# Kernel optimization log

Measured on AMD Instinct MI355X. Metric: run time of the kernel, lower is better.

Reference implementation:

```python
import jax, jax.numpy as jnp
from jax import lax
import numpy as np

B, C, H, W = 8, 256, 192, 192
ATT_K = 11
BN_EPS = 1e-5


def _dwconv(x, w, pad, stride=1):
    # x: NCHW, w: (C,1,kh,kw) depthwise
    return lax.conv_general_dilated(
        x, w, window_strides=(stride, stride), padding=pad,
        feature_group_count=x.shape[1],
        dimension_numbers=('NCHW', 'OIHW', 'NCHW'))


def _max_pool_3x3(x):
    return lax.reduce_window(x, -jnp.inf, lax.max,
                             (1, 1, 3, 3), (1, 1, 1, 1), 'SAME')


def _blur_pool(x, stride=3):
    # antialiased_cnns.BlurPool, filt_size=4: reflect pad [1,2,1,2], binomial 4x4, depthwise, stride 3
    c = x.shape[1]
    a = jnp.array([1., 3., 3., 1.], dtype=x.dtype)
    filt = (a[:, None] * a[None, :])
    filt = filt / jnp.sum(filt)
    w = jnp.tile(filt[None, None], (c, 1, 1, 1))  # (C,1,4,4)
    xp = jnp.pad(x, ((0, 0), (0, 0), (1, 2), (1, 2)), mode='reflect')
    return _dwconv(xp, w, 'VALID', stride=stride)


def _h_transform(x):
    b, c, h, w = x.shape
    x = jnp.pad(x, ((0, 0), (0, 0), (0, 0), (0, w)))
    x = x.reshape(b, c, -1)[..., :-w]
    return x.reshape(b, c, h, 2 * w - 1)


def _inv_h_transform(x):
    b, c, h, _ = x.shape  # last dim = 2h-1 (requires square)
    x = x.reshape(b, c, -1)
    x = jnp.pad(x, ((0, 0), (0, 0), (0, h)))
    x = x.reshape(b, c, h, 2 * h)
    return x[..., :h]


def _v_transform(x):
    return jnp.transpose(_h_transform(jnp.transpose(x, (0, 1, 3, 2))), (0, 1, 3, 2))


def _inv_v_transform(x):
    return jnp.transpose(_inv_h_transform(jnp.transpose(x, (0, 1, 3, 2))), (0, 1, 3, 2))


def setup_inputs() -> dict:
    key = jax.random.key(0)
    ks = jax.random.split(key, 5)
    pad = ATT_K // 2
    return {
        'x': jax.random.normal(ks[0], (B, C, H, W), dtype=jnp.float32),
        'w_h1': jax.random.normal(ks[1], (C, 1, ATT_K, 3), dtype=jnp.float32) * 0.1,
        'w_v1': jax.random.normal(ks[2], (C, 1, 3, ATT_K), dtype=jnp.float32) * 0.1,
        'w_h2': jax.random.normal(ks[3], (C, 1, ATT_K, 3), dtype=jnp.float32) * 0.1,
        'w_v2': jax.random.normal(ks[4], (C, 1, 3, ATT_K), dtype=jnp.float32) * 0.1,
        'bn_gamma': jnp.ones((C,), dtype=jnp.float32),
        'bn_beta': jnp.zeros((C,), dtype=jnp.float32),
        'bn_mean': jnp.zeros((C,), dtype=jnp.float32),
        'bn_var': jnp.ones((C,), dtype=jnp.float32),
    }


def reference(x, w_h1, w_v1, w_h2, w_v2, bn_gamma, bn_beta, bn_mean, bn_var):
    pad = ATT_K // 2
    b, c, h, w = x.shape

    x_tem = _max_pool_3x3(x)
    x_tem = _blur_pool(x_tem, stride=3)  # (B,C,64,64)

    x_h1 = _dwconv(x_tem, w_h1, ((pad, pad), (1, 1)))
    x_w1 = _dwconv(x_tem, w_v1, ((1, 1), (pad, pad)))

    # h == w (192 == 192): diagonal branch active
    x_h2 = _inv_h_transform(_dwconv(_h_transform(x_tem), w_h2, ((pad, pad), (1, 1))))
    x_w2 = _inv_v_transform(_dwconv(_v_transform(x_tem), w_v2, ((1, 1), (pad, pad))))

    s = x_h1 + x_w1 + x_h2 + x_w2
    # inference BatchNorm2d
    inv = bn_gamma / jnp.sqrt(bn_var + BN_EPS)
    att = (s - bn_mean[None, :, None, None]) * inv[None, :, None, None] + bn_beta[None, :, None, None]

    gate = jax.nn.sigmoid(att)
    # nearest interpolate to (h, w): idx = floor(i * in/out)
    ah, aw = gate.shape[2], gate.shape[3]
    idx_h = (jnp.arange(h) * ah) // h
    idx_w = (jnp.arange(w) * aw) // w
    gate_up = gate[:, :, idx_h][:, :, :, idx_w]

    return x[:, :c] * gate_up
```

## Files before the change

### kernel.cpp

```cpp
#include <hip/hip_runtime.h>
#include <hip/hip_fp16.h>
#include <math.h>

#define BN_EPS 1e-5f

typedef _Float16 f16x8 __attribute__((ext_vector_type(8)));
typedef float    f32x4 __attribute__((ext_vector_type(4)));

__device__ __forceinline__ float max3f(float a, float b, float c) {
    return fmaxf(fmaxf(a, b), c);
}

__global__ __launch_bounds__(512, 8)
void mra_fused(const float* __restrict__ x,
               const float* __restrict__ wh1,
               const float* __restrict__ wv1,
               const float* __restrict__ wh2,
               const float* __restrict__ wv2,
               const float* __restrict__ bng,
               const float* __restrict__ bnb,
               const float* __restrict__ bnm,
               const float* __restrict__ bnv,
               float* __restrict__ out)
{
    __shared__ __align__(16) __half sxp_h[76][88];
    __shared__ __align__(16) __half gate_h[64][72];
    __shared__ __align__(16) __half Tpad[13][48];

    const int plane = blockIdx.x;
    const int c     = plane & 255;
    const int tid   = threadIdx.x;
    const int lane  = tid & 63;
    const int w     = tid >> 6;
    const float* __restrict__ xp = x   + (size_t)plane * 36864;
    float* __restrict__       op = out + (size_t)plane * 36864;

    {
        int* z = (int*)&sxp_h[0][0];
        const int nInt = (76 * 88 * 2) / 4;
        #pragma unroll
        for (int i = 0; i < 7; ++i) {
            const int idx = tid + (i << 9);
            if (idx < nInt) z[idx] = 0;
        }
    }
    {
        const float* __restrict__ wh1p = wh1 + c * 33;
        const float* __restrict__ wv1p = wv1 + c * 33;
        const float* __restrict__ wh2p = wh2 + c * 33;
        const float* __restrict__ wv2p = wv2 + c * 33;
        for (int s = tid; s < 13 * 48; s += 512) {
            const int er = s / 48;
            const int e  = er - 6;
            const int d  = (s - er * 48) - 24;
            float t = 0.f;
            if (e >= -5 && e <= 5 && d >= -1 && d <= 1)
                t += wh1p[(e + 5) * 3 + d + 1];
            if (e >= -5 && e <= 5 && d + e >= -1 && d + e <= 1)
                t += wh2p[(e + 5) * 3 + d + e + 1];
            if (e >= -1 && e <= 1 && d >= -5 && d <= 5)
                t += wv1p[(e + 1) * 11 + d + 5];
            if (d + e >= -1 && d + e <= 1 && d >= -5 && d <= 5)
                t += wv2p[(d + e + 1) * 11 + d + 5];
            Tpad[er][s - er * 48] = __float2half(t);
        }
    }
    __syncthreads();

    {
        const int P0  = w << 3;
        const int r0  = 3 * P0 - 2;
        const int col = 3 * lane;

        float c0r[4], c1r[4], c2r[4];
        auto issue = [&](int k, int s) {
            int r = r0 + k;
            r = r < 0 ? 0 : (r > 191 ? 191 : r);
            const float* rp = xp + r * 192 + col;
            c0r[s] = rp[0]; c1r[s] = rp[1]; c2r[s] = rp[2];
        };
        issue(0, 0); issue(1, 1); issue(2, 2); issue(3, 3);

        float h[3][4];
        float hb[3];
        float hbp = 0.f;

        #pragma unroll
        for (int k = 0; k < 27; ++k) {
            const int s = k & 3;
            const float cc0 = c0r[s], cc1 = c1r[s], cc2 = c2r[s];
            if (k + 4 < 27) issue(k + 4, s);

            float xm2 = __shfl_up(cc1, 1);
            float xm1 = __shfl_up(cc2, 1);
            float xp3 = __shfl_down(cc0, 1);
            if (lane == 0)  xm1 = cc0;
            if (lane == 63) xp3 = cc2;

            const float hm_m1 = max3f(xm2, xm1, cc0);
            const float hm_0  = max3f(xm1, cc0, cc1);
            const float hm_1  = max3f(cc0, cc1, cc2);
            const float hm_2  = max3f(cc1, cc2, xp3);

            float* hk = h[k % 3];
            hk[0] = (lane == 0) ? hm_1 : hm_m1;
            hk[1] = hm_0; hk[2] = hm_1; hk[3] = hm_2;

            if (k >= 2) {
                const float* a = h[(k - 2) % 3];
                const float* b = h[(k - 1) % 3];
                const float* d = h[k % 3];
                const float e4 =
                      0.125f * max3f(a[0], b[0], d[0])
                    + 0.375f * max3f(a[1], b[1], d[1])
                    + 0.375f * max3f(a[2], b[2], d[2])
                    + 0.125f * max3f(a[3], b[3], d[3]);
                if (k == 2) {
                    hbp = e4;
                } else {
                    hb[k % 3] = e4;
                    if (k % 3 == 2) {
                        const int i = (k - 5) / 3;
                        float a_out;
                        if (i == 0 && w == 0)
                            a_out = 0.375f * hb[0] + 0.5f * hb[1] + 0.125f * hb[2];
                        else
                            a_out = 0.125f * hbp + 0.375f * hb[0]
                                  + 0.375f * hb[1] + 0.125f * hb[2];
                        hbp = hb[2];
                        sxp_h[(w << 3) + i + 6][lane + 8] = __float2half(a_out);
                    }
                }
            }
        }
    }
    __syncthreads();

    {
        const int lr = lane & 15;
        const int lg = lane >> 4;
        const int t0 = 2 * w;
        const int P0 = (t0 >> 2) << 4;
        const int Q0a = (t0 & 3) << 4;
        const int Q0b = ((t0 + 1) & 3) << 4;
        const int tb = lg * 8 + 16 - lr;

        f32x4 acc0 = {0.f, 0.f, 0.f, 0.f};
        f32x4 acc1 = {0.f, 0.f, 0.f, 0.f};

        #pragma unroll
        for (int e = -6; e <= 6; ++e) {
            const __half* trow = &Tpad[e + 6][0];
            f16x8 bf;
            #pragma unroll
            for (int j = 0; j < 8; ++j)
                bf[j] = *(const _Float16*)&trow[tb + j];
            const int row = P0 + lr + e + 6;
            const f16x8 a0 = *(const f16x8*)&sxp_h[row][Q0a + lg * 8];
            const f16x8 a1 = *(const f16x8*)&sxp_h[row][Q0b + lg * 8];
            acc0 = __builtin_amdgcn_mfma_f32_16x16x32_f16(a0, bf, acc0, 0, 0, 0);
            acc1 = __builtin_amdgcn_mfma_f32_16x16x32_f16(a1, bf, acc1, 0, 0, 0);
        }

        const float inv = bng[c] * rsqrtf(bnv[c] + BN_EPS);
        const float mu  = bnm[c];
        const float bt  = bnb[c];
        #pragma unroll
        for (int r = 0; r < 4; ++r) {
            const int gr = P0 + lg * 4 + r;
            const float g0 = 1.0f / (1.0f + __expf(-((acc0[r] - mu) * inv + bt)));
            const float g1 = 1.0f / (1.0f + __expf(-((acc1[r] - mu) * inv + bt)));
            gate_h[gr][Q0a + lr] = __float2half(g0);
            gate_h[gr][Q0b + lr] = __float2half(g1);
        }
    }
    __syncthreads();

    const float4* __restrict__ x4 = (const float4*)xp + w * 1152;
    float4* __restrict__       o4 = (float4*)op       + w * 1152;
    int rlj[3], gcj[3], rrj[3];
    #pragma unroll
    for (int j = 0; j < 3; ++j) {
        const int idx0 = lane + (j << 6);
        const int rw   = idx0 / 48;
        const int c4   = idx0 - rw * 48;
        rlj[j] = rw;
        const int jb = c4 << 2;
        gcj[j] = jb / 3;
        rrj[j] = jb - 3 * gcj[j];
    }
    #pragma unroll
    for (int u = 0; u < 6; ++u) {
        #pragma unroll
        for (int j = 0; j < 3; ++j) {
            const int row_l = rlj[j] + (u << 2);
            const int idx   = lane + ((u * 3 + j) << 6);
            const int gr    = (w << 3) + row_l / 3;
            const float g0 = __half2float(gate_h[gr][gcj[j]]);
            const float g1 = __half2float(gate_h[gr][gcj[j] + 1]);
            const float4 xv = x4[idx];
            float4 ov;
            const float s1 = (rrj[j] == 2) ? g1 : g0;
            const float s2 = (rrj[j] >= 1) ? g1 : g0;
            ov.x = xv.x * g0;
            ov.y = xv.y * s1;
            ov.z = xv.z * s2;
            ov.w = xv.w * g1;
            o4[idx] = ov;
        }
    }
}

extern "C" void kernel_launch(void* const* d_in, const int* in_sizes, int n_in,
                              void* d_out, int out_size, void* d_ws, size_t ws_size,
                              hipStream_t stream) {
    const float* x   = (const float*)d_in[0];
    const float* wh1 = (const float*)d_in[1];
    const float* wv1 = (const float*)d_in[2];
    const float* wh2 = (const float*)d_in[3];
    const float* wv2 = (const float*)d_in[4];
    const float* g   = (const float*)d_in[5];
    const float* b   = (const float*)d_in[6];
    const float* m   = (const float*)d_in[7];
    const float* v   = (const float*)d_in[8];

    mra_fused<<<dim3(8 * 256), dim3(512), 0, stream>>>(
        x, wh1, wv1, wh2, wv2, g, b, m, v, (float*)d_out);
}
```

Before: 163.8 us.

## Split fused kernel into gate-compute and gate-apply kernels via workspace

Splits the single fused kernel into two. The first computes the pooled conv gates per plane and writes them as fp16 to a global workspace. The second kernel reloads those gates and multiplies them over x, visiting planes in reverse order so the most recently read planes are more likely still in cache. The aim is to decouple the compute-heavy gate phase from the bandwidth-bound apply phase, at the cost of an extra launch, a workspace round-trip, and reading x twice. The old fused kernel stays as a fallback when the workspace is too small.

```diff
diff --git a/kernel.cpp b/kernel.cpp
--- a/kernel.cpp
+++ b/kernel.cpp
@@ -12,7 +12,7 @@
 }
 
 __global__ __launch_bounds__(512, 8)
-void mra_fused(const float* __restrict__ x,
+void mra_gates(const float* __restrict__ x,
                const float* __restrict__ wh1,
                const float* __restrict__ wv1,
                const float* __restrict__ wh2,
@@ -21,10 +21,10 @@
                const float* __restrict__ bnb,
                const float* __restrict__ bnm,
                const float* __restrict__ bnv,
-               float* __restrict__ out)
+               uint32_t* __restrict__ gws)
 {
     __shared__ __align__(16) __half sxp_h[76][88];
-    __shared__ __align__(16) __half gate_h[64][72];
+    __shared__ __align__(16) __half gate_d[64][64];
     __shared__ __align__(16) __half Tpad[13][48];
 
     const int plane = blockIdx.x;
@@ -32,8 +32,7 @@
     const int tid   = threadIdx.x;
     const int lane  = tid & 63;
     const int w     = tid >> 6;
-    const float* __restrict__ xp = x   + (size_t)plane * 36864;
-    float* __restrict__       op = out + (size_t)plane * 36864;
+    const float* __restrict__ xp = x + (size_t)plane * 36864;
 
     {
         int* z = (int*)&sxp_h[0][0];
@@ -140,10 +139,238 @@
         const int lr = lane & 15;
         const int lg = lane >> 4;
         const int t0 = 2 * w;
-        const int P0 = (t0 >> 2) << 4;
+        const int P0  = (t0 >> 2) << 4;
         const int Q0a = (t0 & 3) << 4;
         const int Q0b = ((t0 + 1) & 3) << 4;
-        const int tb = lg * 8 + 16 - lr;
+        const int tb  = lg * 8 + 16 - lr;
+
+        f32x4 acc0 = {0.f, 0.f, 0.f, 0.f};
+        f32x4 acc1 = {0.f, 0.f, 0.f, 0.f};
+
+        #pragma unroll
+        for (int e = -6; e <= 6; ++e) {
+            const __half* trow = &Tpad[e + 6][0];
+            f16x8 bf;
+            #pragma unroll
+            for (int j = 0; j < 8; ++j)
+                bf[j] = *(const _Float16*)&trow[tb + j];
+            const int row = P0 + lr + e + 6;
+            const f16x8 a0 = *(const f16x8*)&sxp_h[row][Q0a + lg * 8];
+            const f16x8 a1 = *(const f16x8*)&sxp_h[row][Q0b + lg * 8];
+            acc0 = __builtin_amdgcn_mfma_f32_16x16x32_f16(a0, bf, acc0, 0, 0, 0);
+            acc1 = __builtin_amdgcn_mfma_f32_16x16x32_f16(a1, bf, acc1, 0, 0, 0);
+        }
+
+        const float inv = bng[c] * rsqrtf(bnv[c] + BN_EPS);
+        const float mu  = bnm[c];
+        const float bt  = bnb[c];
+        #pragma unroll
+        for (int r = 0; r < 4; ++r) {
+            const int gr = P0 + lg * 4 + r;
+            const float g0 = 1.0f / (1.0f + __expf(-((acc0[r] - mu) * inv + bt)));
+            const float g1 = 1.0f / (1.0f + __expf(-((acc1[r] - mu) * inv + bt)));
+            gate_d[gr][Q0a + lr] = __float2half(g0);
+            gate_d[gr][Q0b + lr] = __float2half(g1);
+        }
+    }
+    __syncthreads();
+
+    {
+        const uint32_t* gu = (const uint32_t*)&gate_d[0][0];
+        uint32_t* gp = gws + (size_t)plane * 2048;
+        #pragma unroll
+        for (int i = 0; i < 4; ++i) gp[tid + (i << 9)] = gu[tid + (i << 9)];
+    }
+}
+
+__global__ __launch_bounds__(256, 8)
+void mra_apply(const float* __restrict__ x,
+               const uint32_t* __restrict__ gws,
+               float* __restrict__ out)
+{
+    __shared__ __align__(16) __half gate_l[64][64];
+
+    const int plane = 2047 - blockIdx.x;
+    const int tid   = threadIdx.x;
+    const float* __restrict__ xp = x   + (size_t)plane * 36864;
+    float* __restrict__       op = out + (size_t)plane * 36864;
+
+    {
+        uint32_t* gl = (uint32_t*)&gate_l[0][0];
+        const uint32_t* gp = gws + (size_t)plane * 2048;
+        #pragma unroll
+        for (int i = 0; i < 8; ++i) gl[tid + (i << 8)] = gp[tid + (i << 8)];
+    }
+    __syncthreads();
+
+    const float4* __restrict__ x4 = (const float4*)xp;
+    float4* __restrict__       o4 = (float4*)op;
+    int rowj[3], gcj[3], rrj[3];
+    #pragma unroll
+    for (int j = 0; j < 3; ++j) {
+        const int idx0 = tid + (j << 8);
+        const int rw   = idx0 / 48;
+        const int c4   = idx0 - rw * 48;
+        rowj[j] = rw;
+        const int jb = c4 << 2;
+        gcj[j] = jb / 3;
+        rrj[j] = jb - 3 * gcj[j];
+    }
+    #pragma unroll
+    for (int m = 0; m < 12; ++m) {
+        #pragma unroll
+        for (int j = 0; j < 3; ++j) {
+            const int row = rowj[j] + (m << 4);
+            const int idx = tid + ((m * 3 + j) << 8);
+            const int gr  = row / 3;
+            const float g0 = __half2float(gate_l[gr][gcj[j]]);
+            const float g1 = __half2float(gate_l[gr][gcj[j] + 1]);
+            const float4 xv = x4[idx];
+            float4 ov;
+            const float s1 = (rrj[j] == 2) ? g1 : g0;
+            const float s2 = (rrj[j] >= 1) ? g1 : g0;
+            ov.x = xv.x * g0;
+            ov.y = xv.y * s1;
+            ov.z = xv.z * s2;
+            ov.w = xv.w * g1;
+            o4[idx] = ov;
+        }
+    }
+}
+
+__global__ __launch_bounds__(512, 8)
+void mra_fused(const float* __restrict__ x,
+               const float* __restrict__ wh1,
+               const float* __restrict__ wv1,
+               const float* __restrict__ wh2,
+               const float* __restrict__ wv2,
+               const float* __restrict__ bng,
+               const float* __restrict__ bnb,
+               const float* __restrict__ bnm,
+               const float* __restrict__ bnv,
+               float* __restrict__ out)
+{
+    __shared__ __align__(16) __half sxp_h[76][88];
+    __shared__ __align__(16) __half gate_h[64][72];
+    __shared__ __align__(16) __half Tpad[13][48];
+
+    const int plane = blockIdx.x;
+    const int c     = plane & 255;
+    const int tid   = threadIdx.x;
+    const int lane  = tid & 63;
+    const int w     = tid >> 6;
+    const float* __restrict__ xp = x   + (size_t)plane * 36864;
+    float* __restrict__       op = out + (size_t)plane * 36864;
+
+    {
+        int* z = (int*)&sxp_h[0][0];
+        const int nInt = (76 * 88 * 2) / 4;
+        #pragma unroll
+        for (int i = 0; i < 7; ++i) {
+            const int idx = tid + (i << 9);
+            if (idx < nInt) z[idx] = 0;
+        }
+    }
+    {
+        const float* __restrict__ wh1p = wh1 + c * 33;
+        const float* __restrict__ wv1p = wv1 + c * 33;
+        const float* __restrict__ wh2p = wh2 + c * 33;
+        const float* __restrict__ wv2p = wv2 + c * 33;
+        for (int s = tid; s < 13 * 48; s += 512) {
+            const int er = s / 48;
+            const int e  = er - 6;
+            const int d  = (s - er * 48) - 24;
+            float t = 0.f;
+            if (e >= -5 && e <= 5 && d >= -1 && d <= 1)
+                t += wh1p[(e + 5) * 3 + d + 1];
+            if (e >= -5 && e <= 5 && d + e >= -1 && d + e <= 1)
+                t += wh2p[(e + 5) * 3 + d + e + 1];
+            if (e >= -1 && e <= 1 && d >= -5 && d <= 5)
+                t += wv1p[(e + 1) * 11 + d + 5];
+            if (d + e >= -1 && d + e <= 1 && d >= -5 && d <= 5)
+                t += wv2p[(d + e + 1) * 11 + d + 5];
+            Tpad[er][s - er * 48] = __float2half(t);
+        }
+    }
+    __syncthreads();
+
+    {
+        const int P0  = w << 3;
+        const int r0  = 3 * P0 - 2;
+        const int col = 3 * lane;
+
+        float c0r[4], c1r[4], c2r[4];
+        auto issue = [&](int k, int s) {
+            int r = r0 + k;
+            r = r < 0 ? 0 : (r > 191 ? 191 : r);
+            const float* rp = xp + r * 192 + col;
+            c0r[s] = rp[0]; c1r[s] = rp[1]; c2r[s] = rp[2];
+        };
+        issue(0, 0); issue(1, 1); issue(2, 2); issue(3, 3);
+
+        float h[3][4];
+        float hb[3];
+        float hbp = 0.f;
+
+        #pragma unroll
+        for (int k = 0; k < 27; ++k) {
+            const int s = k & 3;
+            const float cc0 = c0r[s], cc1 = c1r[s], cc2 = c2r[s];
+            if (k + 4 < 27) issue(k + 4, s);
+
+            float xm2 = __shfl_up(cc1, 1);
+            float xm1 = __shfl_up(cc2, 1);
+            float xp3 = __shfl_down(cc0, 1);
+            if (lane == 0)  xm1 = cc0;
+            if (lane == 63) xp3 = cc2;
+
+            const float hm_m1 = max3f(xm2, xm1, cc0);
+            const float hm_0  = max3f(xm1, cc0, cc1);
+            const float hm_1  = max3f(cc0, cc1, cc2);
+            const float hm_2  = max3f(cc1, cc2, xp3);
+
+            float* hk = h[k % 3];
+            hk[0] = (lane == 0) ? hm_1 : hm_m1;
+            hk[1] = hm_0; hk[2] = hm_1; hk[3] = hm_2;
+
+            if (k >= 2) {
+                const float* a = h[(k - 2) % 3];
+                const float* b = h[(k - 1) % 3];
+                const float* d = h[k % 3];
+                const float e4 =
+                      0.125f * max3f(a[0], b[0], d[0])
+                    + 0.375f * max3f(a[1], b[1], d[1])
+                    + 0.375f * max3f(a[2], b[2], d[2])
+                    + 0.125f * max3f(a[3], b[3], d[3]);
+                if (k == 2) {
+                    hbp = e4;
+                } else {
+                    hb[k % 3] = e4;
+                    if (k % 3 == 2) {
+                        const int i = (k - 5) / 3;
+                        float a_out;
+                        if (i == 0 && w == 0)
+                            a_out = 0.375f * hb[0] + 0.5f * hb[1] + 0.125f * hb[2];
+                        else
+                            a_out = 0.125f * hbp + 0.375f * hb[0]
+                                  + 0.375f * hb[1] + 0.125f * hb[2];
+                        hbp = hb[2];
+                        sxp_h[(w << 3) + i + 6][lane + 8] = __float2half(a_out);
+                    }
+                }
+            }
+        }
+    }
+    __syncthreads();
+
+    {
+        const int lr = lane & 15;
+        const int lg = lane >> 4;
+        const int t0 = 2 * w;
+        const int P0  = (t0 >> 2) << 4;
+        const int Q0a = (t0 & 3) << 4;
+        const int Q0b = ((t0 + 1) & 3) << 4;
+        const int tb  = lg * 8 + 16 - lr;
 
         f32x4 acc0 = {0.f, 0.f, 0.f, 0.f};
         f32x4 acc1 = {0.f, 0.f, 0.f, 0.f};
@@ -224,6 +451,15 @@
     const float* m   = (const float*)d_in[7];
     const float* v   = (const float*)d_in[8];
 
-    mra_fused<<<dim3(8 * 256), dim3(512), 0, stream>>>(
-        x, wh1, wv1, wh2, wv2, g, b, m, v, (float*)d_out);
+    const size_t gate_bytes = (size_t)2048 * 2048 * 4;
+    if (ws_size >= gate_bytes) {
+        uint32_t* gws = (uint32_t*)d_ws;
+        mra_gates<<<dim3(2048), dim3(512), 0, stream>>>(
+            x, wh1, wv1, wh2, wv2, g, b, m, v, gws);
+        mra_apply<<<dim3(2048), dim3(256), 0, stream>>>(
+            x, gws, (float*)d_out);
+    } else {
+        mra_fused<<<dim3(2048), dim3(512), 0, stream>>>(
+            x, wh1, wv1, wh2, wv2, g, b, m, v, (float*)d_out);
+    }
 }
```

Measured after the change: 186.2 us. +13.7%, slower.
